# Kernel optimization log

Measured on AMD Instinct MI355X. Metric: run time of the kernel, lower is better.

Reference implementation:

```python
import jax, jax.numpy as jnp
import numpy as np

WS = 8        # window_size
SS = 4        # shift_size
HEADS = 4
DH = 32       # dim_head
SCALE = DH ** -0.5


def setup_inputs() -> dict:
    key = jax.random.key(0)
    k1, k2, k3 = jax.random.split(key, 3)
    B, C, H, W = 8, 128, 256, 256
    inner = HEADS * DH
    x = jax.random.normal(k1, (B, C, H, W), dtype=jnp.float32)
    w_qkv = jax.random.normal(k2, (C, 3 * inner), dtype=jnp.float32) * (C ** -0.5)
    w_proj = jax.random.normal(k3, (inner, C), dtype=jnp.float32) * (inner ** -0.5)
    b_proj = jnp.zeros((C,), dtype=jnp.float32)
    return {"x": x, "w_qkv": w_qkv, "w_proj": w_proj, "b_proj": b_proj}


def reference(x, w_qkv, w_proj, b_proj):
    B, C, H, W = x.shape
    # to channels-last and cyclic shift
    xh = jnp.transpose(x, (0, 2, 3, 1))                      # [B,H,W,C]
    xh = jnp.roll(xh, shift=(-SS, -SS), axis=(1, 2))
    # window partition -> [nW, ws*ws, C]
    nH, nW = H // WS, W // WS
    xw = xh.reshape(B, nH, WS, nW, WS, C)
    xw = jnp.transpose(xw, (0, 1, 3, 2, 4, 1 + 4)).reshape(B * nH * nW, WS * WS, C)
    # qkv
    qkv = xw @ w_qkv                                         # [nWin, L, 3*inner]
    q, k, v = jnp.split(qkv, 3, axis=-1)
    def heads(t):
        n, L, _ = t.shape
        return jnp.transpose(t.reshape(n, L, HEADS, DH), (0, 2, 1, 3))  # [n,h,L,dh]
    q, k, v = heads(q), heads(k), heads(v)
    attn = jax.nn.softmax(jnp.einsum('nhld,nhmd->nhlm', q, k) * SCALE, axis=-1)
    out = jnp.einsum('nhlm,nhmd->nhld', attn, v)             # [n,h,L,dh]
    n, _, L, _ = out.shape
    out = jnp.transpose(out, (0, 2, 1, 3)).reshape(n, L, HEADS * DH)
    out = out @ w_proj + b_proj                              # [n,L,C]
    # window reverse -> [B,H,W,C]
    out = out.reshape(B, nH, nW, WS, WS, C)
    out = jnp.transpose(out, (0, 1, 3, 2, 4, 5)).reshape(B, H, W, C)
    # reverse cyclic shift, back to channels-first
    out = jnp.roll(out, shift=(SS, SS), axis=(1, 2))
    return jnp.transpose(out, (0, 3, 1, 2))                  # [B,C,H,W]
```

## Files before the change

kernel.cpp:

```cpp
#include <hip/hip_runtime.h>


typedef __attribute__((ext_vector_type(8))) short bf16x8;
typedef __attribute__((ext_vector_type(4))) float f32x4;

__device__ __forceinline__ unsigned pk2(float lo, float hi) {
  union { float f; unsigned u; } a, b; a.f = lo; b.f = hi;
  return __builtin_amdgcn_perm(b.u + 0x8000u, a.u + 0x8000u, 0x07060302u);
}

__device__ __forceinline__ unsigned short f2bf_rne(float f) {
  union { float f; unsigned u; } v; v.f = f;
  return (unsigned short)((v.u + 0x7FFFu + ((v.u >> 16) & 1u)) >> 16);
}

__global__ void prep_kernel(const float* __restrict__ wqkv,
                            const float* __restrict__ wproj,
                            unsigned short* __restrict__ wT) {
  const int idx = blockIdx.x * 256 + (int)threadIdx.x;
  if (idx < 384 * 128) {
    const int n = idx >> 7, k = idx & 127;
    wT[idx] = f2bf_rne(wqkv[k * 384 + n]);
  } else {
    const int j = idx - 384 * 128;
    const int n = j >> 7, k = j & 127;
    wT[idx] = f2bf_rne(wproj[k * 128 + n]);
  }
}

__global__ void __launch_bounds__(256, 4)
swin_kernel(const float* __restrict__ x, const unsigned short* __restrict__ wT,
            const float* __restrict__ bproj, float* __restrict__ out) {
  __shared__ unsigned short SM[16384];

  const int bid = blockIdx.x;
  const int win = (bid & 7) * 1024 + (bid >> 3);
  const int b  = win >> 10;
  const int wy = (win >> 5) & 31;
  const int wx = win & 31;
  const int tid  = (int)threadIdx.x;
  const int lane = tid & 63;
  const int wv   = tid >> 6;
  const int q    = lane >> 4;
  const int l16  = lane & 15;
  const int qh   = q >> 1, ql = q & 1;

  unsigned short* XF  = SM;
  unsigned short* SCh = SM + 8192 + wv * 2048;
  unsigned short* QFh = XF + wv * 2048;

  {
    const int t4 = tid & 15;
    const int a  = tid >> 4;
    const int ty = t4 >> 1, txb = (t4 & 1) << 2;
    const int hh = (wy * 8 + ty + 4) & 255;
    const int ww = (wx * 8 + txb + 4) & 255;
    const float* src = x + ((b * 128) * 256 + hh) * 256 + ww;
    const int t0 = t4 << 2;
#pragma unroll
    for (int i = 0; i < 2; ++i) {
      const int c0 = a * 4 + i * 64;
      const float4 v0 = *(const float4*)(src + (c0    ) * 65536);
      const float4 v1 = *(const float4*)(src + (c0 + 1) * 65536);
      const float4 v2 = *(const float4*)(src + (c0 + 2) * 65536);
      const float4 v3 = *(const float4*)(src + (c0 + 3) * 65536);
      unsigned short* p = &XF[(c0 >> 3) * 512 + t0 * 8 + (c0 & 7)];
      uint2 w;
      w.x = pk2(v0.x, v1.x); w.y = pk2(v2.x, v3.x);
      *(uint2*)(p + 0)  = w;
      w.x = pk2(v0.y, v1.y); w.y = pk2(v2.y, v3.y);
      *(uint2*)(p + 8)  = w;
      w.x = pk2(v0.z, v1.z); w.y = pk2(v2.z, v3.z);
      *(uint2*)(p + 16) = w;
      w.x = pk2(v0.w, v1.w); w.y = pk2(v2.w, v3.w);
      *(uint2*)(p + 24) = w;
    }
  }
  __syncthreads();

  f32x4 aQT[2][4] = {}; f32x4 aKT[2][4] = {};
#pragma unroll
  for (int ks = 0; ks < 4; ++ks) {
    const int ko = ks * 32 + q * 8;
    bf16x8 xb[4];
#pragma unroll
    for (int nt = 0; nt < 4; ++nt)
      xb[nt] = *(const bf16x8*)&XF[(ks * 4 + q) * 512 + (nt * 16 + l16) * 8];
#pragma unroll
    for (int mA = 0; mA < 2; ++mA) {
      const int row = wv * 32 + mA * 16 + l16;
      const bf16x8 wq = *(const bf16x8*)&wT[row * 128 + ko];
      const bf16x8 wk = *(const bf16x8*)&wT[(128 + row) * 128 + ko];
      __builtin_amdgcn_s_setprio(1);
#pragma unroll
      for (int nt = 0; nt < 4; ++nt) {
        aQT[mA][nt] = __builtin_amdgcn_mfma_f32_16x16x32_bf16(wq, xb[nt], aQT[mA][nt], 0, 0, 0);
        aKT[mA][nt] = __builtin_amdgcn_mfma_f32_16x16x32_bf16(wk, xb[nt], aKT[mA][nt], 0, 0, 0);
      }
      __builtin_amdgcn_s_setprio(0);
    }
  }
#pragma unroll
  for (int mA = 0; mA < 2; ++mA)
#pragma unroll
    for (int nt = 0; nt < 4; ++nt) {
      uint2 w;
      w.x = pk2(aKT[mA][nt][0], aKT[mA][nt][1]);
      w.y = pk2(aKT[mA][nt][2], aKT[mA][nt][3]);
      *(uint2*)&SCh[(mA * 2 + qh) * 512 + (nt * 16 + l16) * 8 + ql * 4] = w;
    }
  bf16x8 kf[4];
#pragma unroll
  for (int t = 0; t < 4; ++t)
    kf[t] = *(const bf16x8*)&SCh[q * 512 + (t * 16 + l16) * 8];
  asm volatile("" ::: "memory");

  f32x4 aV[4][2] = {};
#pragma unroll
  for (int ks = 0; ks < 4; ++ks) {
    const int ko = ks * 32 + q * 8;
    bf16x8 af[4];
#pragma unroll
    for (int mt = 0; mt < 4; ++mt)
      af[mt] = *(const bf16x8*)&XF[(ks * 4 + q) * 512 + (mt * 16 + l16) * 8];
#pragma unroll
    for (int nt = 0; nt < 2; ++nt) {
      const bf16x8 bv = *(const bf16x8*)&wT[(256 + wv * 32 + nt * 16 + l16) * 128 + ko];
      __builtin_amdgcn_s_setprio(1);
#pragma unroll
      for (int mt = 0; mt < 4; ++mt)
        aV[mt][nt] = __builtin_amdgcn_mfma_f32_16x16x32_bf16(af[mt], bv, aV[mt][nt], 0, 0, 0);
      __builtin_amdgcn_s_setprio(0);
    }
  }
#pragma unroll
  for (int mt = 0; mt < 4; ++mt)
#pragma unroll
    for (int nt = 0; nt < 2; ++nt) {
      uint2 w;
      w.x = pk2(aV[mt][nt][0], aV[mt][nt][1]);
      w.y = pk2(aV[mt][nt][2], aV[mt][nt][3]);
      *(uint2*)&SCh[(mt * 2 + qh) * 256 + (nt * 16 + l16) * 8 + ql * 4] = w;
    }
  __syncthreads();

  constexpr float SC = 0.17677669529663687f * 1.4426950408889634f;
#pragma unroll
  for (int mA = 0; mA < 2; ++mA)
#pragma unroll
    for (int nt = 0; nt < 4; ++nt) {
      uint2 w;
      w.x = pk2(aQT[mA][nt][0] * SC, aQT[mA][nt][1] * SC);
      w.y = pk2(aQT[mA][nt][2] * SC, aQT[mA][nt][3] * SC);
      *(uint2*)&QFh[(mA * 2 + qh) * 512 + (nt * 16 + l16) * 8 + ql * 4] = w;
    }
  bf16x8 qf[4];
#pragma unroll
  for (int t = 0; t < 4; ++t)
    qf[t] = *(const bf16x8*)&QFh[q * 512 + (t * 16 + l16) * 8];

  f32x4 aOT[2][4] = {};
  float sacc[4] = {0.f, 0.f, 0.f, 0.f};
#pragma unroll
  for (int h = 0; h < 2; ++h) {
    f32x4 aSh[2][4] = {};
    __builtin_amdgcn_s_setprio(1);
#pragma unroll
    for (int mh = 0; mh < 2; ++mh)
#pragma unroll
      for (int nt = 0; nt < 4; ++nt)
        aSh[mh][nt] = __builtin_amdgcn_mfma_f32_16x16x32_bf16(kf[h * 2 + mh], qf[nt], aSh[mh][nt], 0, 0, 0);
    __builtin_amdgcn_s_setprio(0);
#pragma unroll
    for (int mh = 0; mh < 2; ++mh)
#pragma unroll
      for (int nt = 0; nt < 4; ++nt) {
#pragma unroll
        for (int r = 0; r < 4; ++r)
          aSh[mh][nt][r] = __builtin_amdgcn_exp2f(aSh[mh][nt][r]);
        sacc[nt] += aSh[mh][nt][0] + aSh[mh][nt][1] + aSh[mh][nt][2] + aSh[mh][nt][3];
        uint2 w;
        w.x = pk2(aSh[mh][nt][0], aSh[mh][nt][1]);
        w.y = pk2(aSh[mh][nt][2], aSh[mh][nt][3]);
        *(uint2*)&QFh[(mh * 2 + qh) * 512 + (nt * 16 + l16) * 8 + ql * 4] = w;
      }
    bf16x8 pf[4], vf[2];
#pragma unroll
    for (int t = 0; t < 4; ++t)
      pf[t] = *(const bf16x8*)&QFh[q * 512 + (t * 16 + l16) * 8];
#pragma unroll
    for (int nb = 0; nb < 2; ++nb)
      vf[nb] = *(const bf16x8*)&SCh[(h * 4 + q) * 256 + (nb * 16 + l16) * 8];
    __builtin_amdgcn_s_setprio(1);
#pragma unroll
    for (int mo = 0; mo < 2; ++mo)
#pragma unroll
      for (int np = 0; np < 4; ++np)
        aOT[mo][np] = __builtin_amdgcn_mfma_f32_16x16x32_bf16(vf[mo], pf[np], aOT[mo][np], 0, 0, 0);
    __builtin_amdgcn_s_setprio(0);
  }
  float inv[4];
#pragma unroll
  for (int nt = 0; nt < 4; ++nt) {
    float s = sacc[nt];
    s += __shfl_xor(s, 16);
    s += __shfl_xor(s, 32);
    inv[nt] = 1.0f / s;
  }

#pragma unroll
  for (int mo = 0; mo < 2; ++mo)
#pragma unroll
    for (int np = 0; np < 4; ++np) {
      const float s = inv[np];
      uint2 w;
      w.x = pk2(aOT[mo][np][0] * s, aOT[mo][np][1] * s);
      w.y = pk2(aOT[mo][np][2] * s, aOT[mo][np][3] * s);
      *(uint2*)&XF[(wv * 4 + mo * 2 + qh) * 512 + (np * 16 + l16) * 8 + ql * 4] = w;
    }
  __syncthreads();

  f32x4 aP[4][2] = {};
#pragma unroll
  for (int ks = 0; ks < 4; ++ks) {
    const int ko = ks * 32 + q * 8;
    bf16x8 af[4];
#pragma unroll
    for (int mt = 0; mt < 4; ++mt)
      af[mt] = *(const bf16x8*)&XF[(ks * 4 + q) * 512 + (mt * 16 + l16) * 8];
#pragma unroll
    for (int nt = 0; nt < 2; ++nt) {
      const bf16x8 bw = *(const bf16x8*)&wT[(384 + wv * 32 + nt * 16 + l16) * 128 + ko];
      __builtin_amdgcn_s_setprio(1);
#pragma unroll
      for (int mt = 0; mt < 4; ++mt)
        aP[mt][nt] = __builtin_amdgcn_mfma_f32_16x16x32_bf16(af[mt], bw, aP[mt][nt], 0, 0, 0);
      __builtin_amdgcn_s_setprio(0);
    }
  }
#pragma unroll
  for (int nt = 0; nt < 2; ++nt) {
    const int c = wv * 32 + nt * 16 + l16;
    const float bias = bproj[c];
#pragma unroll
    for (int mt = 0; mt < 4; ++mt) {
      const int tb  = mt * 16 + q * 4;
      const int ty  = tb >> 3;
      const int txb = tb & 7;
      const int hh  = (wy * 8 + ty + 4) & 255;
      const int ww  = (wx * 8 + txb + 4) & 255;
      float4 v;
      v.x = aP[mt][nt][0] + bias;
      v.y = aP[mt][nt][1] + bias;
      v.z = aP[mt][nt][2] + bias;
      v.w = aP[mt][nt][3] + bias;
      *(float4*)(out + ((b * 128 + c) * 256 + hh) * 256 + ww) = v;
    }
  }
}

extern "C" void kernel_launch(void* const* d_in, const int* in_sizes, int n_in,
                              void* d_out, int out_size, void* d_ws, size_t ws_size,
                              hipStream_t stream) {
  const float* x     = (const float*)d_in[0];
  const float* wqkv  = (const float*)d_in[1];
  const float* wproj = (const float*)d_in[2];
  const float* bp    = (const float*)d_in[3];
  unsigned short* wT = (unsigned short*)d_ws;

  prep_kernel<<<256, 256, 0, stream>>>(wqkv, wproj, wT);
  swin_kernel<<<8192, 256, 0, stream>>>(x, wT, bp, (float*)d_out);
}
```

Measured before the change: 607.8 us.

## Fuse V projection into QK loop, prefetch weights, move Q buffer to own LDS

Computes the V projection inside the same k-loop as Q and K so the X fragments are loaded from LDS once. The first k-slice of the weights is prefetched before the first barrier and the projection weights before attention, which hides some global-load latency. Q gets its own LDS region, so one barrier can move to just before the output is written back over XF. The cost is a larger LDS footprint (48KB) and more live registers, with launch bounds lowered from 4 to 3 blocks per CU, which may reduce occupancy.

Result: no change. 602.4 us (-0.9%).

```diff
diff --git a/kernel.cpp b/kernel.cpp
--- a/kernel.cpp
+++ b/kernel.cpp
@@ -28,10 +28,10 @@
   }
 }
 
-__global__ void __launch_bounds__(256, 4)
+__global__ void __launch_bounds__(256, 3)
 swin_kernel(const float* __restrict__ x, const unsigned short* __restrict__ wT,
             const float* __restrict__ bproj, float* __restrict__ out) {
-  __shared__ unsigned short SM[16384];
+  __shared__ unsigned short SM[24576];
 
   const int bid = blockIdx.x;
   const int win = (bid & 7) * 1024 + (bid >> 3);
@@ -46,8 +46,8 @@
   const int qh   = q >> 1, ql = q & 1;
 
   unsigned short* XF  = SM;
-  unsigned short* SCh = SM + 8192 + wv * 2048;
-  unsigned short* QFh = XF + wv * 2048;
+  unsigned short* SCh = SM + 8192  + wv * 2048;
+  unsigned short* QFh = SM + 16384 + wv * 2048;
 
   {
     const int t4 = tid & 15;
@@ -76,9 +76,23 @@
       *(uint2*)(p + 24) = w;
     }
   }
+
+  bf16x8 wq0[2], wk0[2], bv0[2];
+  {
+    const int ko0 = q * 8;
+#pragma unroll
+    for (int mA = 0; mA < 2; ++mA) {
+      const int row = wv * 32 + mA * 16 + l16;
+      wq0[mA] = *(const bf16x8*)&wT[row * 128 + ko0];
+      wk0[mA] = *(const bf16x8*)&wT[(128 + row) * 128 + ko0];
+    }
+#pragma unroll
+    for (int nt = 0; nt < 2; ++nt)
+      bv0[nt] = *(const bf16x8*)&wT[(256 + wv * 32 + nt * 16 + l16) * 128 + ko0];
+  }
   __syncthreads();
 
-  f32x4 aQT[2][4] = {}; f32x4 aKT[2][4] = {};
+  f32x4 aQT[2][4] = {}; f32x4 aKT[2][4] = {}; f32x4 aV[4][2] = {};
 #pragma unroll
   for (int ks = 0; ks < 4; ++ks) {
     const int ko = ks * 32 + q * 8;
@@ -86,20 +100,42 @@
 #pragma unroll
     for (int nt = 0; nt < 4; ++nt)
       xb[nt] = *(const bf16x8*)&XF[(ks * 4 + q) * 512 + (nt * 16 + l16) * 8];
+    bf16x8 wq[2], wk[2], bv[2];
+    if (ks == 0) {
+      wq[0] = wq0[0]; wq[1] = wq0[1];
+      wk[0] = wk0[0]; wk[1] = wk0[1];
+      bv[0] = bv0[0]; bv[1] = bv0[1];
+    } else {
+#pragma unroll
+      for (int mA = 0; mA < 2; ++mA) {
+        const int row = wv * 32 + mA * 16 + l16;
+        wq[mA] = *(const bf16x8*)&wT[row * 128 + ko];
+        wk[mA] = *(const bf16x8*)&wT[(128 + row) * 128 + ko];
+      }
+#pragma unroll
+      for (int nt = 0; nt < 2; ++nt)
+        bv[nt] = *(const bf16x8*)&wT[(256 + wv * 32 + nt * 16 + l16) * 128 + ko];
+    }
 #pragma unroll
     for (int mA = 0; mA < 2; ++mA) {
-      const int row = wv * 32 + mA * 16 + l16;
-      const bf16x8 wq = *(const bf16x8*)&wT[row * 128 + ko];
-      const bf16x8 wk = *(const bf16x8*)&wT[(128 + row) * 128 + ko];
       __builtin_amdgcn_s_setprio(1);
 #pragma unroll
       for (int nt = 0; nt < 4; ++nt) {
-        aQT[mA][nt] = __builtin_amdgcn_mfma_f32_16x16x32_bf16(wq, xb[nt], aQT[mA][nt], 0, 0, 0);
-        aKT[mA][nt] = __builtin_amdgcn_mfma_f32_16x16x32_bf16(wk, xb[nt], aKT[mA][nt], 0, 0, 0);
+        aQT[mA][nt] = __builtin_amdgcn_mfma_f32_16x16x32_bf16(wq[mA], xb[nt], aQT[mA][nt], 0, 0, 0);
+        aKT[mA][nt] = __builtin_amdgcn_mfma_f32_16x16x32_bf16(wk[mA], xb[nt], aKT[mA][nt], 0, 0, 0);
       }
       __builtin_amdgcn_s_setprio(0);
     }
-  }
+#pragma unroll
+    for (int nt = 0; nt < 2; ++nt) {
+      __builtin_amdgcn_s_setprio(1);
+#pragma unroll
+      for (int mt = 0; mt < 4; ++mt)
+        aV[mt][nt] = __builtin_amdgcn_mfma_f32_16x16x32_bf16(xb[mt], bv[nt], aV[mt][nt], 0, 0, 0);
+      __builtin_amdgcn_s_setprio(0);
+    }
+  }
+
 #pragma unroll
   for (int mA = 0; mA < 2; ++mA)
 #pragma unroll
@@ -115,24 +151,6 @@
     kf[t] = *(const bf16x8*)&SCh[q * 512 + (t * 16 + l16) * 8];
   asm volatile("" ::: "memory");
 
-  f32x4 aV[4][2] = {};
-#pragma unroll
-  for (int ks = 0; ks < 4; ++ks) {
-    const int ko = ks * 32 + q * 8;
-    bf16x8 af[4];
-#pragma unroll
-    for (int mt = 0; mt < 4; ++mt)
-      af[mt] = *(const bf16x8*)&XF[(ks * 4 + q) * 512 + (mt * 16 + l16) * 8];
-#pragma unroll
-    for (int nt = 0; nt < 2; ++nt) {
-      const bf16x8 bv = *(const bf16x8*)&wT[(256 + wv * 32 + nt * 16 + l16) * 128 + ko];
-      __builtin_amdgcn_s_setprio(1);
-#pragma unroll
-      for (int mt = 0; mt < 4; ++mt)
-        aV[mt][nt] = __builtin_amdgcn_mfma_f32_16x16x32_bf16(af[mt], bv, aV[mt][nt], 0, 0, 0);
-      __builtin_amdgcn_s_setprio(0);
-    }
-  }
 #pragma unroll
   for (int mt = 0; mt < 4; ++mt)
 #pragma unroll
@@ -142,7 +160,6 @@
       w.y = pk2(aV[mt][nt][2], aV[mt][nt][3]);
       *(uint2*)&SCh[(mt * 2 + qh) * 256 + (nt * 16 + l16) * 8 + ql * 4] = w;
     }
-  __syncthreads();
 
   constexpr float SC = 0.17677669529663687f * 1.4426950408889634f;
 #pragma unroll
@@ -158,6 +175,11 @@
 #pragma unroll
   for (int t = 0; t < 4; ++t)
     qf[t] = *(const bf16x8*)&QFh[q * 512 + (t * 16 + l16) * 8];
+
+  bf16x8 bw0[2];
+#pragma unroll
+  for (int nt = 0; nt < 2; ++nt)
+    bw0[nt] = *(const bf16x8*)&wT[(384 + wv * 32 + nt * 16 + l16) * 128 + q * 8];
 
   f32x4 aOT[2][4] = {};
   float sacc[4] = {0.f, 0.f, 0.f, 0.f};
@@ -208,6 +230,8 @@
     inv[nt] = 1.0f / s;
   }
 
+  __syncthreads();
+
 #pragma unroll
   for (int mo = 0; mo < 2; ++mo)
 #pragma unroll
@@ -230,7 +254,9 @@
       af[mt] = *(const bf16x8*)&XF[(ks * 4 + q) * 512 + (mt * 16 + l16) * 8];
 #pragma unroll
     for (int nt = 0; nt < 2; ++nt) {
-      const bf16x8 bw = *(const bf16x8*)&wT[(384 + wv * 32 + nt * 16 + l16) * 128 + ko];
+      bf16x8 bw;
+      if (ks == 0) bw = bw0[nt];
+      else bw = *(const bf16x8*)&wT[(384 + wv * 32 + nt * 16 + l16) * 128 + ko];
       __builtin_amdgcn_s_setprio(1);
 #pragma unroll
       for (int mt = 0; mt < 4; ++mt)
```
